# Optimization experiments

Measured on AMD Instinct MI355X. Metric: run time of the kernel, lower is better.

The kernel has to match this reference:

```python
import jax, jax.numpy as jnp
import numpy as np

B, K, H_IMG, W_IMG = 8, 1, 512, 512
N_ITR = 10      # fixed iteration count (torch max_itr loop, unrolled via scan)
TOL = 1e-3      # convergence tolerance used for per-element gating


def setup_inputs() -> dict:
    key = jax.random.key(0)
    k1, k2 = jax.random.split(key)
    img = jax.random.normal(k1, (B, K, H_IMG, W_IMG), dtype=jnp.float32)
    temp = jax.random.normal(k2, (B, K, H_IMG, W_IMG), dtype=jnp.float32)
    return {"img": img, "temp": temp}


def _grad_batch(F):
    # central difference with replicate padding (== conv with [-0.5,0,0.5])
    px = jnp.pad(F, ((0, 0), (0, 0), (0, 0), (1, 1)), mode='edge')
    dx = 0.5 * (px[..., 2:] - px[..., :-2])
    py = jnp.pad(F, ((0, 0), (0, 0), (1, 1), (0, 0)), mode='edge')
    dy = 0.5 * (py[..., 2:, :] - py[..., :-2, :])
    return dx, dy


def _bilinear_sample(img, xp, yp):
    # img [B,k,h,w]; xp,yp pixel coords [B,h,w]; zeros padding, align_corners=True
    _, k, h, w = img.shape
    x0 = jnp.floor(xp)
    y0 = jnp.floor(yp)
    wx1 = xp - x0
    wy1 = yp - y0

    def tap(xi, yi, wgt):
        valid = (xi >= 0) & (xi <= w - 1) & (yi >= 0) & (yi <= h - 1)
        xc = jnp.clip(xi, 0, w - 1).astype(jnp.int32)
        yc = jnp.clip(yi, 0, h - 1).astype(jnp.int32)
        v = jax.vmap(lambda im, yy, xx: im[:, yy, xx])(img, yc, xc)  # [B,k,h,w]
        return v * (wgt * valid.astype(img.dtype))[:, None]

    return (tap(x0, y0, (1 - wx1) * (1 - wy1)) + tap(x0 + 1, y0, wx1 * (1 - wy1))
            + tap(x0, y0 + 1, (1 - wx1) * wy1) + tap(x0 + 1, y0 + 1, wx1 * wy1))


def _deeplk(img, temp):
    Bb, k, h, w = temp.shape
    gx, gy = _grad_batch(temp)
    # centered pixel coordinates (meshgrid with x - x.max()/2)
    xs = jnp.arange(w, dtype=jnp.float32) - (w - 1) / 2.0
    ys = jnp.arange(h, dtype=jnp.float32) - (h - 1) / 2.0
    X, Y = jnp.meshgrid(xs, ys)  # each [h,w]
    Xf = jnp.tile(X.reshape(-1), k)  # [k*h*w]
    Yf = jnp.tile(Y.reshape(-1), k)
    gxf = gx.reshape(Bb, -1)
    gyf = gy.reshape(Bb, -1)
    # Jacobian dI/dp: [B, k*h*w, 8]
    dIdp = jnp.stack([
        Xf * gxf, Yf * gxf, gxf,
        Xf * gyf, Yf * gyf, gyf,
        -Xf * Xf * gxf - Xf * Yf * gyf,
        -Xf * Yf * gxf - Yf * Yf * gyf], axis=-1)
    Hm = jnp.einsum('bni,bnj->bij', dIdp, dIdp)        # [B,8,8]
    invH = jnp.linalg.inv(Hm)
    invH_dIdp = jnp.einsum('bij,bnj->bin', invH, dIdp)  # [B,8,N]

    xy1 = jnp.stack([X.reshape(-1), Y.reshape(-1),
                     jnp.ones(h * w, jnp.float32)], axis=0)  # [3, h*w]
    I3 = jnp.eye(3, dtype=jnp.float32)

    def param_to_H(p):
        return I3 + jnp.concatenate([p, jnp.zeros((Bb, 1), p.dtype)], 1).reshape(Bb, 3, 3)

    def step(carry, _):
        p, dp = carry  # p,dp: [B,8]
        Hh = param_to_H(p)
        xyw = jnp.einsum('bij,jn->bin', Hh, xy1)
        Xw = (xyw[:, 0] / xyw[:, 2]).reshape(Bb, h, w) + (w - 1) / 2.0
        Yw = (xyw[:, 1] / xyw[:, 2]).reshape(Bb, h, w) + (h - 1) / 2.0
        Fi_warp = _bilinear_sample(img, Xw, Yw)
        xn = Xw / ((w - 1) / 2.0) - 1.0
        yn = Yw / ((h - 1) / 2.0) - 1.0
        mask = ((xn > -1 + 2.0 / w) & (xn < 1 - 2.0 / w) &
                (yn > -1 + 2.0 / h) & (yn < 1 - 2.0 / h)).astype(img.dtype)
        r = (Fi_warp - temp * mask[:, None]).reshape(Bb, -1)  # [B,N]
        dp_new = jnp.einsum('bin,bn->bi', invH_dIdp, r)       # [B,8]
        dp_new = dp_new.at[:, 6:8].set(0.0)                   # no projective update
        gate = (jnp.linalg.norm(dp, axis=1, keepdims=True) > TOL).astype(p.dtype)
        dp_next = gate * dp_new
        return (p - dp_next, dp_next), None

    p0 = jnp.zeros((Bb, 8), jnp.float32)
    dp0 = jnp.ones((Bb, 8), jnp.float32)
    (p, _), _ = jax.lax.scan(step, (p0, dp0), None, length=N_ITR)
    return p.reshape(Bb, 8, 1), param_to_H(p)


def reference(img, temp):
    return _deeplk(img, temp)
```

## Files before the change

kernel.cpp:

```cpp
#include <hip/hip_runtime.h>
#include <math.h>

#define W     512
#define HH    512
#define NB    8
#define NBLK  512
#define TPB   512
#define NW    (TPB / 64)
#define BPB   64
#define ROWS  8
#define NPX   (ROWS * W)
#define PXT   (NPX / TPB)
#define NITR  10
#define POISON64 0xAAAAAAAAAAAAAAAAull
#define ALL64  0xFFFFFFFFFFFFFFFFull
#define MLO 0.998046875f
#define MHI 510.001953125f

__device__ __forceinline__ float wave_reduce8(float x) {
    x += __shfl_down(x, 32, 64);
    x += __shfl_down(x, 16, 64);
    x += __shfl_down(x, 8, 64);
    return x;
}
__device__ __forceinline__ double load_d(const double* p) {
    unsigned long long u = __hip_atomic_load((const unsigned long long*)p,
                       __ATOMIC_RELAXED, __HIP_MEMORY_SCOPE_AGENT);
    return __builtin_bit_cast(double, u);
}
__device__ __forceinline__ void store_d(double* p, double v) {
    __hip_atomic_store((unsigned long long*)p, __builtin_bit_cast(unsigned long long, v),
                       __ATOMIC_RELAXED, __HIP_MEMORY_SCOPE_AGENT);
}
__device__ __forceinline__ bool not_poison(double v) {
    return __builtin_bit_cast(unsigned long long, v) != POISON64;
}

__device__ __forceinline__ float hrec(int t, float X1, float X2, float X3, float X4,
    float a0, float a1, float a2, float b0, float b1, float b2, float b3,
    float c0, float c1, float c2, float c3, float c4)
{
    switch (t) {
    case 0:  return X2 * a0;             case 1:  return X1 * a1;
    case 2:  return X1 * a0;             case 3:  return X2 * b0;
    case 4:  return X1 * b1;             case 5:  return X1 * b0;
    case 6:  return -(X3 * a0 + X2 * b1);
    case 7:  return -(X2 * a1 + X1 * b2);
    case 8:  return a2;                  case 9:  return a1;
    case 10: return X1 * b1;             case 11: return b2;
    case 12: return b1;
    case 13: return -(X2 * a1 + X1 * b2);
    case 14: return -(X1 * a2 + b3);
    case 15: return a0;                  case 16: return X1 * b0;
    case 17: return b1;                  case 18: return b0;
    case 19: return -(X2 * a0 + X1 * b1);
    case 20: return -(X1 * a1 + b2);
    case 21: return X2 * c0;             case 22: return X1 * c1;
    case 23: return X1 * c0;
    case 24: return -(X3 * b0 + X2 * c1);
    case 25: return -(X2 * b1 + X1 * c2);
    case 26: return c2;                  case 27: return c1;
    case 28: return -(X2 * b1 + X1 * c2);
    case 29: return -(X1 * b2 + c3);
    case 30: return c0;
    case 31: return -(X2 * b0 + X1 * c1);
    case 32: return -(X1 * b1 + c2);
    case 33: return X4 * a0 + 2.f * X3 * b1 + X2 * c2;
    case 34: return X3 * a1 + 2.f * X2 * b2 + X1 * c3;
    default: return X2 * a2 + 2.f * X1 * b3 + c4;
    }
}

extern "C" __global__ __launch_bounds__(TPB, 4)
void deeplk_kernel(const float* __restrict__ img, const float* __restrict__ temp,
                   float* __restrict__ out, void* __restrict__ wsv)
{
    double* Hpart = (double*)wsv;
    double* vpart = Hpart + NB * 36 * BPB;

    const int tid   = threadIdx.x;
    const int lane  = tid & 63;
    const int wv    = tid >> 6;
    const int b     = blockIdx.x & 7;
    const int chunk = blockIdx.x >> 3;
    const int row0  = chunk * ROWS;
    const float* tb = temp + b * (HH * W);
    const float* ib = img  + b * (HH * W);

    __shared__ float  s_gx[NPX], s_gy[NPX], s_tv[NPX];
    __shared__ float  s_h8[64 * 36];
    __shared__ float  s_h2[8 * 36];
    __shared__ double s_Hu[36];
    __shared__ double s_invH[64];
    __shared__ double s_p[8], s_dp[8], s_v[8];
    __shared__ double s_vred[8 * 8];

    const float X1 = (float)tid - 255.5f;

    float a0 = 0.f, a1 = 0.f, a2 = 0.f;
    float b0 = 0.f, b1 = 0.f, b2 = 0.f, b3 = 0.f;
    float c0 = 0.f, c1 = 0.f, c2 = 0.f, c3 = 0.f, c4 = 0.f;
    float A = 0.f, Bv = 0.f, Cv = 0.f, Dv = 0.f, Ev = 0.f;
    {
        const int cc = tid;
        const int cl = (cc > 0) ? cc - 1 : 0;
        const int cr = (cc < W - 1) ? cc + 1 : W - 1;
        const bool xm = (cc >= 1) && (cc <= 510);
        float Yv = (float)row0 - 255.5f;
#pragma unroll
        for (int u = 0; u < PXT; ++u) {
            const int i  = tid + u * TPB;
            const int rr = row0 + u;
            const int ru = (rr > 0) ? rr - 1 : 0;
            const int rd = (rr < HH - 1) ? rr + 1 : HH - 1;
            const float gx = 0.5f * (tb[rr * W + cr] - tb[rr * W + cl]);
            const float gy = 0.5f * (tb[rd * W + cc] - tb[ru * W + cc]);
            const float tc = tb[rr * W + cc];
            s_gx[i] = gx; s_gy[i] = gy; s_tv[i] = tc;
            const float q1 = gx * gx, q2 = gx * gy, q3 = gy * gy;
            const float y2 = Yv * Yv, y3 = y2 * Yv, y4 = y2 * y2;
            a0 += q1; a1 += Yv * q1; a2 += y2 * q1;
            b0 += q2; b1 += Yv * q2; b2 += y2 * q2; b3 += y3 * q2;
            c0 += q3; c1 += Yv * q3; c2 += y2 * q3; c3 += y3 * q3; c4 += y4 * q3;
            const float m  = (xm && rr >= 1 && rr <= 510) ? 1.f : 0.f;
            const float rv = ib[rr * W + cc] - tc * m;
            const float t1 = gx * rv, t2 = gy * rv;
            A  += t1;        Bv += t2;
            Cv += Yv * t1;   Dv += Yv * t2;
            Ev += y2 * t2;
            Yv += 1.f;
        }
    }
    {
        const float X2 = X1 * X1, X3 = X2 * X1, X4 = X2 * X2;
#pragma unroll
        for (int t = 0; t < 36; ++t) {
            float x = wave_reduce8(hrec(t, X1, X2, X3, X4,
                                        a0, a1, a2, b0, b1, b2, b3,
                                        c0, c1, c2, c3, c4));
            if (lane < 8) s_h8[(wv * 8 + lane) * 36 + t] = x;
        }
        __syncthreads();
        if (tid < 288) {
            const int g = tid / 36, t = tid % 36;
            float s = 0.f;
#pragma unroll
            for (int w2 = 0; w2 < 8; ++w2) s += s_h8[(w2 * 8 + g) * 36 + t];
            s_h2[g * 36 + t] = s;
        }
        __syncthreads();
        if (tid < 36) {
            double s = 0.0;
#pragma unroll
            for (int g = 0; g < 8; ++g) s += (double)s_h2[g * 36 + tid];
            store_d(&Hpart[(b * 36 + tid) * BPB + chunk], s);
        }
        __syncthreads();
        float va[8];
        va[0] = X1 * A;  va[1] = Cv;  va[2] = A;
        va[3] = X1 * Bv; va[4] = Dv;  va[5] = Bv;
        va[6] = -(X2 * A + X1 * Dv);
        va[7] = -(X1 * Cv + Ev);
#pragma unroll
        for (int c = 0; c < 8; ++c) {
            float x = wave_reduce8(va[c]);
            if (lane < 8) s_h8[(wv * 8 + lane) * 8 + c] = x;
        }
        __syncthreads();
        if (tid < 64) {
            const int g = tid >> 3, c = tid & 7;
            float s = 0.f;
#pragma unroll
            for (int w2 = 0; w2 < 8; ++w2) s += s_h8[(w2 * 8 + g) * 8 + c];
            s_h2[g * 8 + c] = s;
        }
        __syncthreads();
        if (tid < 8) {
            double s = 0.0;
#pragma unroll
            for (int g = 0; g < 8; ++g) s += (double)s_h2[g * 8 + tid];
            store_d(&vpart[b * BPB * 8 + chunk * 8 + tid], s);
        }
    }
    for (int c = wv; c < 36; c += NW) {
        const double* hp = &Hpart[(b * 36 + c) * BPB + lane];
        double x;
        for (;;) {
            x = load_d(hp);
            if (__ballot(not_poison(x)) == ALL64) break;
            __builtin_amdgcn_s_sleep(1);
        }
        x += __shfl_down(x, 32, 64);
        x += __shfl_down(x, 16, 64);
        x += __shfl_down(x, 8, 64);
        x += __shfl_down(x, 4, 64);
        x += __shfl_down(x, 2, 64);
        x += __shfl_down(x, 1, 64);
        if (lane == 0) s_Hu[c] = x;
    }
    {
        const double* slot = &vpart[b * BPB * 8 + tid];
        double x;
        for (;;) {
            x = load_d(slot);
            if (__ballot(not_poison(x)) == ALL64) break;
            __builtin_amdgcn_s_sleep(1);
        }
        x += __shfl_down(x, 32, 64);
        x += __shfl_down(x, 16, 64);
        x += __shfl_down(x, 8, 64);
        if (lane < 8) s_vred[wv * 8 + lane] = x;
    }
    __syncthreads();
    if (tid < 8) {
        double s = 0.0;
#pragma unroll
        for (int w2 = 0; w2 < NW; ++w2) s += s_vred[w2 * 8 + tid];
        s_v[tid] = s;
    }
    __syncthreads();

    if (tid < 64) {
        const int r  = tid >> 3, cj = tid & 7;
        const int i2 = (r < cj) ? r : cj;
        const int j2 = (r < cj) ? cj : r;
        double a = s_Hu[i2 * 8 - (i2 * (i2 - 1)) / 2 + (j2 - i2)];
        double e = (r == cj) ? 1.0 : 0.0;
#pragma unroll
        for (int k = 0; k < 8; ++k) {
            int pr = k;
            double pv = fabs(__shfl(a, k * 8 + k, 64));
            for (int rr2 = k + 1; rr2 < 8; ++rr2) {
                double c = fabs(__shfl(a, rr2 * 8 + k, 64));
                if (c > pv) { pv = c; pr = rr2; }
            }
            double a_k = __shfl(a, k * 8 + cj, 64),  e_k = __shfl(e, k * 8 + cj, 64);
            double a_p = __shfl(a, pr * 8 + cj, 64), e_p = __shfl(e, pr * 8 + cj, 64);
            if (r == k)       { a = a_p; e = e_p; }
            else if (r == pr) { a = a_k; e = e_k; }
            double piv = __shfl(a, k * 8 + k, 64);
            double d = 1.0 / piv;
            if (r == k) { a *= d; e *= d; }
            double f  = __shfl(a, r * 8 + k, 64);
            double ak = __shfl(a, k * 8 + cj, 64);
            double ek = __shfl(e, k * 8 + cj, 64);
            if (r != k) { a -= f * ak; e -= f * ek; }
        }
        s_invH[tid] = e;
    }
    __syncthreads();
    if (tid < 8) {
        double dpn = 0.0;
#pragma unroll
        for (int l = 0; l < 8; ++l) dpn += s_invH[tid * 8 + l] * s_v[l];
        if (tid >= 6) dpn = 0.0;
        s_p[tid]  = -dpn;
        s_dp[tid] = dpn;
    }
    __syncthreads();

    for (int it = 1; it < NITR; ++it) {
        double n2 = 0.0;
#pragma unroll
        for (int l = 0; l < 8; ++l) { double d = s_dp[l]; n2 += d * d; }
        if (n2 > 1e-6) {
            const float a00 = 1.f + (float)s_p[0];
            const float a01 = (float)s_p[1];
            const float a02 = (float)s_p[2] + 255.5f;
            const float a10 = (float)s_p[3];
            const float a11 = 1.f + (float)s_p[4];
            const float a12 = (float)s_p[5] + 255.5f;
            float Yv = (float)row0 - 255.5f;
            float Xw = a00 * X1 + a01 * Yv + a02;
            float Yw = a10 * X1 + a11 * Yv + a12;
            float Ai = 0.f, Bi = 0.f, Ci = 0.f, Di = 0.f, Ei = 0.f;

#pragma unroll
            for (int u = 0; u < PXT; ++u) {
                const int i = tid + u * TPB;
                const float xf = floorf(Xw), yf = floorf(Yw);
                const int ix = (int)xf, iy = (int)yf;
                const float wx = Xw - xf, wy = Yw - yf;
                const bool vx0 = (ix >= 0) & (ix < W);
                const bool vx1 = (ix >= -1) & (ix < W - 1);
                const bool vy0 = (iy >= 0) & (iy < HH);
                const bool vy1 = (iy >= -1) & (iy < HH - 1);
                const float* ro0 = ib + iy * W;
                const float* ro1 = ro0 + W;
                const float t00 = (vx0 && vy0) ? ro0[ix]     : 0.f;
                const float t10 = (vx1 && vy0) ? ro0[ix + 1] : 0.f;
                const float t01 = (vx0 && vy1) ? ro1[ix]     : 0.f;
                const float t11 = (vx1 && vy1) ? ro1[ix + 1] : 0.f;
                const float omx = 1.f - wx, omy = 1.f - wy;
                const float Fi = (t00 * omx + t10 * wx) * omy
                               + (t01 * omx + t11 * wx) * wy;
                const float m = (Xw > MLO && Xw < MHI && Yw > MLO && Yw < MHI) ? 1.f : 0.f;
                const float rv = Fi - s_tv[i] * m;
                const float t1 = s_gx[i] * rv, t2 = s_gy[i] * rv;
                Ai += t1;        Bi += t2;
                Ci += Yv * t1;   Di += Yv * t2;
                Ei += (Yv * Yv) * t2;
                Xw += a01; Yw += a11; Yv += 1.f;
            }
            float va[8];
            {
                const float X2 = X1 * X1;
                va[0] = X1 * Ai; va[1] = Ci;  va[2] = Ai;
                va[3] = X1 * Bi; va[4] = Di;  va[5] = Bi;
                va[6] = -(X2 * Ai + X1 * Di);
                va[7] = -(X1 * Ci + Ei);
            }
#pragma unroll
            for (int c = 0; c < 8; ++c) {
                float x = wave_reduce8(va[c]);
                if (lane < 8) s_h8[(wv * 8 + lane) * 8 + c] = x;
            }
            __syncthreads();
            if (tid < 64) {
                const int g = tid >> 3, c = tid & 7;
                float s = 0.f;
#pragma unroll
                for (int w2 = 0; w2 < 8; ++w2) s += s_h8[(w2 * 8 + g) * 8 + c];
                s_h2[g * 8 + c] = s;
            }
            __syncthreads();
            double* vp = vpart + ((it * NB) + b) * BPB * 8;
            if (tid < 8) {
                double s = 0.0;
#pragma unroll
                for (int g = 0; g < 8; ++g) s += (double)s_h2[g * 8 + tid];
                store_d(&vp[chunk * 8 + tid], s);
            }
            {
                const double* slot = &vp[tid];
                double x;
                for (;;) {
                    x = load_d(slot);
                    if (__ballot(not_poison(x)) == ALL64) break;
                    __builtin_amdgcn_s_sleep(1);
                }
                x += __shfl_down(x, 32, 64);
                x += __shfl_down(x, 16, 64);
                x += __shfl_down(x, 8, 64);
                if (lane < 8) s_vred[wv * 8 + lane] = x;
            }
            __syncthreads();
            if (tid < 8) {
                double s = 0.0;
#pragma unroll
                for (int w2 = 0; w2 < NW; ++w2) s += s_vred[w2 * 8 + tid];
                s_v[tid] = s;
            }
            __syncthreads();
            if (tid < 8) {
                double dpn = 0.0;
#pragma unroll
                for (int l = 0; l < 8; ++l) dpn += s_invH[tid * 8 + l] * s_v[l];
                if (tid >= 6) dpn = 0.0;
                s_p[tid] -= dpn;
                s_dp[tid] = dpn;
            }
            __syncthreads();
        }
    }

    if (chunk == 0) {
        if (tid < 8) out[b * 8 + tid] = (float)s_p[tid];
        if (tid == 0) {
            float* Ho = out + 64 + b * 9;
            Ho[0] = 1.f + (float)s_p[0]; Ho[1] = (float)s_p[1];       Ho[2] = (float)s_p[2];
            Ho[3] = (float)s_p[3];       Ho[4] = 1.f + (float)s_p[4]; Ho[5] = (float)s_p[5];
            Ho[6] = (float)s_p[6];       Ho[7] = (float)s_p[7];       Ho[8] = 1.f;
        }
    }
}

extern "C" void kernel_launch(void* const* d_in, const int* in_sizes, int n_in,
                              void* d_out, int out_size, void* d_ws, size_t ws_size,
                              hipStream_t stream) {
    const float* img  = (const float*)d_in[0];
    const float* temp = (const float*)d_in[1];
    float* out = (float*)d_out;
    void*  ws  = d_ws;
    void* args[] = { &img, &temp, &out, &ws };
    hipError_t e = hipLaunchCooperativeKernel((const void*)deeplk_kernel, dim3(NBLK),
                                              dim3(TPB), args, 0, stream);
    if (e != hipSuccess) {
        deeplk_kernel<<<dim3(NBLK), dim3(TPB), 0, stream>>>(img, temp, out, ws);
    }
}
```

Measured before the change: 152.4 us.

## Collapse per-iteration vector reduction into one wave and drop block barriers

The cross-block partial sums for the 8-element residual vector are now stored column-major and gathered by a single wave, which polls all 8 components at once, reduces them with shuffles and computes the parameter update in-wave. This removes several __syncthreads barriers per Gauss-Newton iteration and the separate s_v staging step, shortening the serial latency chain in this persistent, grid-synchronised kernel. The spin loop no longer sleeps, which may raise memory polling traffic, and correctness depends on an explicit vmcnt wait and on intra-wave ordering of shared memory accesses.

```diff
diff --git a/kernel.cpp b/kernel.cpp
--- a/kernel.cpp
+++ b/kernel.cpp
@@ -18,6 +18,12 @@
 #define MHI 510.001953125f
 
 __device__ __forceinline__ float wave_reduce8(float x) {
+    x += __shfl_down(x, 32, 64);
+    x += __shfl_down(x, 16, 64);
+    x += __shfl_down(x, 8, 64);
+    return x;
+}
+__device__ __forceinline__ double red8_d(double x) {
     x += __shfl_down(x, 32, 64);
     x += __shfl_down(x, 16, 64);
     x += __shfl_down(x, 8, 64);
@@ -92,8 +98,8 @@
     __shared__ float  s_h2[8 * 36];
     __shared__ double s_Hu[36];
     __shared__ double s_invH[64];
-    __shared__ double s_p[8], s_dp[8], s_v[8];
-    __shared__ double s_vred[8 * 8];
+    __shared__ double s_p[8], s_dp[8];
+    __shared__ double s_vred[64];
 
     const float X1 = (float)tid - 255.5f;
 
@@ -155,40 +161,64 @@
             for (int g = 0; g < 8; ++g) s += (double)s_h2[g * 36 + tid];
             store_d(&Hpart[(b * 36 + tid) * BPB + chunk], s);
         }
-        __syncthreads();
         float va[8];
         va[0] = X1 * A;  va[1] = Cv;  va[2] = A;
         va[3] = X1 * Bv; va[4] = Dv;  va[5] = Bv;
-        va[6] = -(X2 * A + X1 * Dv);
+        va[6] = -(X1 * X1 * A + X1 * Dv);
         va[7] = -(X1 * Cv + Ev);
 #pragma unroll
         for (int c = 0; c < 8; ++c) {
             float x = wave_reduce8(va[c]);
             if (lane < 8) s_h8[(wv * 8 + lane) * 8 + c] = x;
         }
+        asm volatile("s_waitcnt vmcnt(0)" ::: "memory");
         __syncthreads();
+    }
+    {
+        double* vc0 = vpart + b * 8 * BPB;
         if (tid < 64) {
-            const int g = tid >> 3, c = tid & 7;
-            float s = 0.f;
-#pragma unroll
-            for (int w2 = 0; w2 < 8; ++w2) s += s_h8[(w2 * 8 + g) * 8 + c];
-            s_h2[g * 8 + c] = s;
+            {
+                const int g = tid >> 3, c = tid & 7;
+                float s = 0.f;
+#pragma unroll
+                for (int w2 = 0; w2 < 8; ++w2) s += s_h8[(w2 * 8 + g) * 8 + c];
+                s_h2[g * 8 + c] = s;
+            }
+            if (tid < 8) {
+                double s = 0.0;
+#pragma unroll
+                for (int g = 0; g < 8; ++g) s += (double)s_h2[g * 8 + tid];
+                store_d(&vc0[tid * BPB + chunk], s);
+            }
+            const double* p0 = vc0 + lane;
+            double x0, x1, x2, x3, x4, x5, x6, x7;
+            for (;;) {
+                x0 = load_d(p0);            x1 = load_d(p0 + BPB);
+                x2 = load_d(p0 + 2 * BPB);  x3 = load_d(p0 + 3 * BPB);
+                x4 = load_d(p0 + 4 * BPB);  x5 = load_d(p0 + 5 * BPB);
+                x6 = load_d(p0 + 6 * BPB);  x7 = load_d(p0 + 7 * BPB);
+                bool ok = not_poison(x0) && not_poison(x1) && not_poison(x2) &&
+                          not_poison(x3) && not_poison(x4) && not_poison(x5) &&
+                          not_poison(x6) && not_poison(x7);
+                if (__ballot(ok) == ALL64) break;
+            }
+            x0 = red8_d(x0); x1 = red8_d(x1); x2 = red8_d(x2); x3 = red8_d(x3);
+            x4 = red8_d(x4); x5 = red8_d(x5); x6 = red8_d(x6); x7 = red8_d(x7);
+            if (lane < 8) {
+                s_vred[0 * 8 + lane] = x0; s_vred[1 * 8 + lane] = x1;
+                s_vred[2 * 8 + lane] = x2; s_vred[3 * 8 + lane] = x3;
+                s_vred[4 * 8 + lane] = x4; s_vred[5 * 8 + lane] = x5;
+                s_vred[6 * 8 + lane] = x6; s_vred[7 * 8 + lane] = x7;
+            }
         }
         __syncthreads();
-        if (tid < 8) {
-            double s = 0.0;
-#pragma unroll
-            for (int g = 0; g < 8; ++g) s += (double)s_h2[g * 8 + tid];
-            store_d(&vpart[b * BPB * 8 + chunk * 8 + tid], s);
-        }
     }
     for (int c = wv; c < 36; c += NW) {
         const double* hp = &Hpart[(b * 36 + c) * BPB + lane];
-        double x;
-        for (;;) {
+        double x = load_d(hp);
+        while (__ballot(not_poison(x)) != ALL64) {
+            __builtin_amdgcn_s_sleep(1);
             x = load_d(hp);
-            if (__ballot(not_poison(x)) == ALL64) break;
-            __builtin_amdgcn_s_sleep(1);
         }
         x += __shfl_down(x, 32, 64);
         x += __shfl_down(x, 16, 64);
@@ -197,26 +227,6 @@
         x += __shfl_down(x, 2, 64);
         x += __shfl_down(x, 1, 64);
         if (lane == 0) s_Hu[c] = x;
-    }
-    {
-        const double* slot = &vpart[b * BPB * 8 + tid];
-        double x;
-        for (;;) {
-            x = load_d(slot);
-            if (__ballot(not_poison(x)) == ALL64) break;
-            __builtin_amdgcn_s_sleep(1);
-        }
-        x += __shfl_down(x, 32, 64);
-        x += __shfl_down(x, 16, 64);
-        x += __shfl_down(x, 8, 64);
-        if (lane < 8) s_vred[wv * 8 + lane] = x;
-    }
-    __syncthreads();
-    if (tid < 8) {
-        double s = 0.0;
-#pragma unroll
-        for (int w2 = 0; w2 < NW; ++w2) s += s_vred[w2 * 8 + tid];
-        s_v[tid] = s;
     }
     __syncthreads();
 
@@ -248,11 +258,13 @@
         }
         s_invH[tid] = e;
     }
-    __syncthreads();
     if (tid < 8) {
+        double v = 0.0;
+#pragma unroll
+        for (int l = 0; l < 8; ++l) v += s_vred[tid * 8 + l];
         double dpn = 0.0;
 #pragma unroll
-        for (int l = 0; l < 8; ++l) dpn += s_invH[tid * 8 + l] * s_v[l];
+        for (int l = 0; l < 8; ++l) dpn += s_invH[tid * 8 + l] * __shfl(v, l, 64);
         if (tid >= 6) dpn = 0.0;
         s_p[tid]  = -dpn;
         s_dp[tid] = dpn;
@@ -316,49 +328,53 @@
                 if (lane < 8) s_h8[(wv * 8 + lane) * 8 + c] = x;
             }
             __syncthreads();
+            double* vp = vpart + ((it * NB) + b) * 8 * BPB;
             if (tid < 64) {
-                const int g = tid >> 3, c = tid & 7;
-                float s = 0.f;
-#pragma unroll
-                for (int w2 = 0; w2 < 8; ++w2) s += s_h8[(w2 * 8 + g) * 8 + c];
-                s_h2[g * 8 + c] = s;
-            }
-            __syncthreads();
-            double* vp = vpart + ((it * NB) + b) * BPB * 8;
-            if (tid < 8) {
-                double s = 0.0;
-#pragma unroll
-                for (int g = 0; g < 8; ++g) s += (double)s_h2[g * 8 + tid];
-                store_d(&vp[chunk * 8 + tid], s);
-            }
-            {
-                const double* slot = &vp[tid];
-                double x;
+                {
+                    const int g = tid >> 3, c = tid & 7;
+                    float s = 0.f;
+#pragma unroll
+                    for (int w2 = 0; w2 < 8; ++w2) s += s_h8[(w2 * 8 + g) * 8 + c];
+                    s_h2[g * 8 + c] = s;
+                }
+                if (tid < 8) {
+                    double s = 0.0;
+#pragma unroll
+                    for (int g = 0; g < 8; ++g) s += (double)s_h2[g * 8 + tid];
+                    store_d(&vp[tid * BPB + chunk], s);
+                }
+                const double* p0 = vp + lane;
+                double x0, x1, x2, x3, x4, x5, x6, x7;
                 for (;;) {
-                    x = load_d(slot);
-                    if (__ballot(not_poison(x)) == ALL64) break;
-                    __builtin_amdgcn_s_sleep(1);
+                    x0 = load_d(p0);            x1 = load_d(p0 + BPB);
+                    x2 = load_d(p0 + 2 * BPB);  x3 = load_d(p0 + 3 * BPB);
+                    x4 = load_d(p0 + 4 * BPB);  x5 = load_d(p0 + 5 * BPB);
+                    x6 = load_d(p0 + 6 * BPB);  x7 = load_d(p0 + 7 * BPB);
+                    bool ok = not_poison(x0) && not_poison(x1) && not_poison(x2) &&
+                              not_poison(x3) && not_poison(x4) && not_poison(x5) &&
+                              not_poison(x6) && not_poison(x7);
+                    if (__ballot(ok) == ALL64) break;
                 }
-                x += __shfl_down(x, 32, 64);
-                x += __shfl_down(x, 16, 64);
-                x += __shfl_down(x, 8, 64);
-                if (lane < 8) s_vred[wv * 8 + lane] = x;
-            }
-            __syncthreads();
-            if (tid < 8) {
-                double s = 0.0;
-#pragma unroll
-                for (int w2 = 0; w2 < NW; ++w2) s += s_vred[w2 * 8 + tid];
-                s_v[tid] = s;
-            }
-            __syncthreads();
-            if (tid < 8) {
-                double dpn = 0.0;
-#pragma unroll
-                for (int l = 0; l < 8; ++l) dpn += s_invH[tid * 8 + l] * s_v[l];
-                if (tid >= 6) dpn = 0.0;
-                s_p[tid] -= dpn;
-                s_dp[tid] = dpn;
+                x0 = red8_d(x0); x1 = red8_d(x1); x2 = red8_d(x2); x3 = red8_d(x3);
+                x4 = red8_d(x4); x5 = red8_d(x5); x6 = red8_d(x6); x7 = red8_d(x7);
+                if (lane < 8) {
+                    s_vred[0 * 8 + lane] = x0; s_vred[1 * 8 + lane] = x1;
+                    s_vred[2 * 8 + lane] = x2; s_vred[3 * 8 + lane] = x3;
+                    s_vred[4 * 8 + lane] = x4; s_vred[5 * 8 + lane] = x5;
+                    s_vred[6 * 8 + lane] = x6; s_vred[7 * 8 + lane] = x7;
+                }
+                if (tid < 8) {
+                    double v = 0.0;
+#pragma unroll
+                    for (int l = 0; l < 8; ++l) v += s_vred[tid * 8 + l];
+                    double dpn = 0.0;
+#pragma unroll
+                    for (int l = 0; l < 8; ++l)
+                        dpn += s_invH[tid * 8 + l] * __shfl(v, l, 64);
+                    if (tid >= 6) dpn = 0.0;
+                    s_p[tid] -= dpn;
+                    s_dp[tid] = dpn;
+                }
             }
             __syncthreads();
         }
```

New measurement: 190.7 us. 25.1% more time.
